# Performance work log

Measured on AMD Instinct MI355X. Metric: run time of the kernel, lower is better.

The kernel has to match this reference:

```python
import jax, jax.numpy as jnp
import numpy as np
from jax import lax

NEG = -1e9
B, H, C, TX, TY = 4, 256, 80, 256, 1024  # batch, hidden, mel bins, text len, mel len


def setup_inputs() -> dict:
    key = jax.random.key(0)
    k = jax.random.split(key, 6)
    en = jax.random.normal(k[0], (B, H, TX), jnp.float32)
    mu = jax.random.normal(k[1], (B, C, TX), jnp.float32)
    log_sigma = 0.1 * jax.random.normal(k[2], (B, C, TX), jnp.float32)
    y = jax.random.normal(k[3], (B, C, TY), jnp.float32)
    x_lengths = jax.random.randint(k[4], (B,), TX // 2, TX + 1, jnp.int32)
    y_lengths = jax.random.randint(k[5], (B,), TY // 2, TY + 1, jnp.int32)
    return {"en": en, "mu": mu, "log_sigma": log_sigma, "y": y,
            "x_lengths": x_lengths, "y_lengths": y_lengths}


def sequence_mask(lengths, max_len):
    return jnp.arange(max_len)[None, :] < lengths[:, None]


def compute_log_probs(mu, log_sigma, y):
    # y: [B,C,Ty] -> [B,1,Ty,C]; mu/log_sigma: [B,C,Tx] -> [B,Tx,1,C]
    yb = jnp.transpose(y, (0, 2, 1))[:, None]
    mub = jnp.transpose(mu, (0, 2, 1))[:, :, None]
    lsb = jnp.transpose(log_sigma, (0, 2, 1))[:, :, None]
    # mse / sigma^2 = (y-mu)^2 * exp(-2*log_sigma); mean over channel dim
    expo = -0.5 * jnp.mean((yb - mub) ** 2 * jnp.exp(-2.0 * lsb), axis=-1)  # [B,Tx,Ty]
    return expo - 0.5 * jnp.mean(lsb, axis=-1)  # broadcast [B,Tx,1] -> [B,Tx,Ty]


def maximum_path(logp, mask, x_lengths, y_lengths):
    """Monotonic alignment search (Glow-TTS Viterbi DP), vectorized over batch."""
    b, tx, ty = logp.shape
    lp = jnp.where(mask > 0, logp, NEG)
    cols = jnp.moveaxis(lp, 2, 0)  # [Ty, B, Tx]
    v0 = jnp.broadcast_to(jnp.where(jnp.arange(tx) == 0, 0.0, NEG), (b, tx)).astype(logp.dtype)

    def fwd(v, col):
        v_shift = jnp.concatenate([jnp.full((b, 1), NEG, v.dtype), v[:, :-1]], axis=1)
        diag = v_shift > v  # come from (x-1, y-1) rather than (x, y-1)
        return col + jnp.maximum(v, v_shift), diag

    _, diags = lax.scan(fwd, v0, cols)  # diags: [Ty, B, Tx] bool

    xs_idx = jnp.arange(tx)

    def bwd(idx, inp):
        yv, dcol = inp
        active = yv < y_lengths  # [B]
        row = (xs_idx[None, :] == idx[:, None]) & active[:, None]
        d = jnp.take_along_axis(dcol, idx[:, None], axis=1)[:, 0]
        idx = jnp.where(active & (idx > 0) & d, idx - 1, idx)
        return idx, row

    _, rows = lax.scan(bwd, x_lengths - 1, (jnp.arange(ty), diags), reverse=True)
    return lax.stop_gradient(jnp.moveaxis(rows, 0, 2).astype(logp.dtype))  # [B,Tx,Ty]


def generate_path(dr, mask):
    # dr: [B,Tx] durations; mask: [B,Tx,Ty]
    ty = mask.shape[-1]
    cum = jnp.cumsum(dr, axis=1)
    pm = (jnp.arange(ty)[None, None, :] < cum[:, :, None]).astype(dr.dtype)
    path = pm - jnp.pad(pm, ((0, 0), (1, 0), (0, 0)))[:, :-1]
    return path * mask


def reference(en, mu, log_sigma, y, x_lengths, y_lengths):
    tx, ty = mu.shape[-1], y.shape[-1]
    x_mask = sequence_mask(x_lengths, tx).astype(jnp.float32)  # [B,Tx]
    y_mask = sequence_mask(y_lengths, ty).astype(jnp.float32)  # [B,Ty]
    attn_mask = x_mask[:, :, None] * y_mask[:, None, :]        # [B,Tx,Ty]
    logp = compute_log_probs(mu, log_sigma, y)
    attn = maximum_path(logp, attn_mask, x_lengths, y_lengths)
    dr_mas = jnp.sum(attn, axis=-1)                            # durations [B,Tx]
    path = generate_path(dr_mas, attn_mask)                    # convert_dr_to_align
    # expand_encoder_outputs: attn^T @ en^T -> [B,H,Ty]
    o_en_ex = jnp.einsum('bxy,bhx->bhy', path, en)
    return o_en_ex, logp, attn, dr_mas
```

## Files before the change

kernel.cpp:

```cpp
#include <hip/hip_runtime.h>
#include <cstdint>
#include <cmath>

#define B_ 4
#define H_ 256
#define C_ 80
#define TX_ 256
#define TY_ 1024
#define NCH_ 32
#define NEGF (-1e9f)

#define OFF_LOGP (B_*H_*TY_)
#define OFF_ATTN (OFF_LOGP + B_*TX_*TY_)
#define OFF_DR   (OFF_ATTN + B_*TX_*TY_)

__device__ __forceinline__ float dpp_shr1_negfill_f32(float x) {
  union { float f; int i; } u, o, r;
  u.f = x; o.f = NEGF;
  r.i = __builtin_amdgcn_update_dpp(o.i, u.i, 0x138, 0xf, 0xf, false);
  return r.f;
}

__global__ __launch_bounds__(256) void k_logp(
    const float* __restrict__ mu, const float* __restrict__ ls,
    const float* __restrict__ y, const int* __restrict__ xlp,
    const int* __restrict__ ylp, float* __restrict__ logp_out,
    float* __restrict__ lpT)
{
  const int b  = blockIdx.y;
  const int x0 = blockIdx.x * 4;
  const int tid = threadIdx.x;
  __shared__ double s_w[4][C_];
  __shared__ double s_m1[4][C_];
  __shared__ double s_wm2[4][C_];
  __shared__ double s_lsv[4][C_];
  __shared__ double s_K[4];
  __shared__ double s_t0[4];
  __shared__ float tile[TY_][4];
  for (int i = tid; i < 4 * C_; i += 256) {
    int xi = i / C_, c = i - xi * C_;
    double m = (double)mu[(b * C_ + c) * TX_ + x0 + xi];
    double l = (double)ls[(b * C_ + c) * TX_ + x0 + xi];
    double w = exp(-2.0 * l);
    s_w[xi][c]   = w;
    s_m1[xi][c]  = -2.0 * w * m;
    s_wm2[xi][c] = w * m * m;
    s_lsv[xi][c] = l;
  }
  __syncthreads();
  {
    int xi = tid >> 6, cc = tid & 63;
    double kp = (cc < C_) ? s_wm2[xi][cc] : 0.0;
    double tp = (cc < C_) ? s_lsv[xi][cc] : 0.0;
    if (cc + 64 < C_) { kp += s_wm2[xi][cc + 64]; tp += s_lsv[xi][cc + 64]; }
#pragma unroll
    for (int off = 32; off; off >>= 1) {
      kp += __shfl_down(kp, off);
      tp += __shfl_down(tp, off);
    }
    if (cc == 0) { s_K[xi] = kp; s_t0[xi] = -0.5 * (tp * (1.0 / C_)); }
  }
  __syncthreads();

  const int t0 = tid * 4;
  double acc[4][4];
#pragma unroll
  for (int xi = 0; xi < 4; ++xi)
#pragma unroll
    for (int k = 0; k < 4; ++k) acc[xi][k] = 0.0;

  const float4* yp = (const float4*)(y + (size_t)b * C_ * TY_) + tid;
#pragma unroll 4
  for (int c = 0; c < C_; ++c) {
    float4 yv = yp[c * (TY_ / 4)];
    double y0 = yv.x, y1 = yv.y, y2 = yv.z, y3 = yv.w;
#pragma unroll
    for (int xi = 0; xi < 4; ++xi) {
      double w = s_w[xi][c], m1 = s_m1[xi][c];
      double u0 = fma(w, y0, m1), u1 = fma(w, y1, m1);
      double u2 = fma(w, y2, m1), u3 = fma(w, y3, m1);
      acc[xi][0] = fma(u0, y0, acc[xi][0]);
      acc[xi][1] = fma(u1, y1, acc[xi][1]);
      acc[xi][2] = fma(u2, y2, acc[xi][2]);
      acc[xi][3] = fma(u3, y3, acc[xi][3]);
    }
  }

  const int xlen = xlp[b], ylen = ylp[b];
#pragma unroll
  for (int xi = 0; xi < 4; ++xi) {
    int x = x0 + xi;
    double c0 = s_t0[xi], K = s_K[xi];
    float r[4];
#pragma unroll
    for (int k = 0; k < 4; ++k)
      r[k] = (float)((acc[xi][k] + K) * (-0.5 / C_) + c0);
    *(float4*)&logp_out[((size_t)(b * TX_ + x)) * TY_ + t0] =
        make_float4(r[0], r[1], r[2], r[3]);
    bool xm = x < xlen;
#pragma unroll
    for (int k = 0; k < 4; ++k)
      tile[t0 + k][xi] = (xm && (t0 + k) < ylen) ? r[k] : NEGF;
  }
  __syncthreads();

  float* dst = lpT + (size_t)b * TY_ * TX_ + x0;
  const float4* tp = (const float4*)tile;
#pragma unroll
  for (int k = 0; k < 4; ++k) {
    int t = tid + 256 * k;
    *(float4*)&dst[(size_t)t * TX_] = tp[t];
  }
}

#define PHASE_BAR() \
  asm volatile("s_waitcnt lgkmcnt(0)\n\ts_barrier" ::: "memory")

#define PHASEQ(FL, FC, q)                                                   \
  {                                                                         \
    const int cl = (q) - w;                                                 \
    const int clc = cl < 0 ? 0 : (cl >= NCH_ ? NCH_ - 1 : cl);              \
    const float* cb = gb + (size_t)clc * 32 * TX_ + tid;                    \
    _Pragma("unroll")                                                       \
    for (int i = 0; i < 32; ++i) FL[i] = cb[i * TX_];    \
    const int cc = (q) - 2 - w;                                             \
    if (cc >= 0 && cc < NCH_) {                                             \
      if (cc == 0) v = (tid == 0) ? 0.0f : NEGF;                            \
      uint32_t word = 0u;                                                   \
      const float* bp = &bdry[cc & 1][w][0];                                \
      float bv[32];                                                         \
      _Pragma("unroll")                                                     \
      for (int i = 0; i < 8; ++i)                                           \
        *(float4*)&bv[4 * i] = *(const float4*)(bp + 4 * i);                \
      float bs[32];                                                         \
      bs[0] = v;                                                            \
      _Pragma("unroll")                                                     \
      for (int i = 0; i < 32; ++i) {                                        \
        float vl = dpp_shr1_negfill_f32(v);                                 \
        if (amlane0) vl = bv[i];                                            \
        if (vl > v) word |= (1u << i);                                      \
        float nv = FC[i] + fmaxf(v, vl);                                    \
        if (i < 31) bs[i + 1] = nv;                                         \
        v = nv;                                                             \
      }                                                                     \
      if (lane == 63) {                                                     \
        float* wr = &bdry[cc & 1][w + 1][0];                                \
        _Pragma("unroll")                                                   \
        for (int i = 0; i < 8; ++i)                                         \
          *(float4*)(wr + 4 * i) = *(float4*)&bs[4 * i];                    \
      }                                                                     \
      bits[cc * 256 + tid] = word;                                          \
    }                                                                       \
    PHASE_BAR();                                                            \
  }

__global__ __launch_bounds__(256, 1) void k_dp(
    const float* __restrict__ lpT, const int* __restrict__ xlp,
    const int* __restrict__ ylp, float* __restrict__ dr_out,
    int* __restrict__ cum_ws, int* __restrict__ xt_ws)
{
  const int b = blockIdx.x;
  const int tid = threadIdx.x;
  const int lane = tid & 63;
  const int w = tid >> 6;
  __shared__ uint32_t bits[8192];
  __shared__ uint32_t dur[TX_];
  __shared__ float bdry[2][5][32];

  const float* gb = lpT + (size_t)b * TY_ * TX_;
  const bool amlane0 = (w > 0) && (lane == 0);

  float v = NEGF;
  float f0[32], f1[32], f2[32];

  for (int q = 0; q < 39; q += 3) {
    PHASEQ(f0, f1, q);
    PHASEQ(f1, f2, q + 1);
    PHASEQ(f2, f0, q + 2);
  }
  __syncthreads();

  dur[tid] = 0;
  __syncthreads();

  const int xlen = xlp[b], ylen = ylp[b];
  if (tid == 0) {
    int idx = xlen - 1;
    int t = ylen - 1;
    while (t >= 0) {
      if (idx == 0) { dur[0] = (uint32_t)(t + 1); break; }
      int ww = t >> 5, rr = t & 31;
      uint32_t w0 = bits[ww * 256 + idx];
      uint32_t w1 = (ww > 0) ? bits[(ww - 1) * 256 + idx] : 0u;
      w0 &= (rr == 31) ? 0xffffffffu : ((1u << (rr + 1)) - 1u);
      uint32_t wd = w0;
      int wsel = ww;
      if (wd == 0) { wd = w1; wsel = ww - 1; }
      while (wd == 0 && wsel > 0) { --wsel; wd = bits[wsel * 256 + idx]; }
      if (wd == 0) { dur[idx] = (uint32_t)(t + 1); break; }
      int bitpos = 31 - __builtin_clz(wd);
      int tp = (wsel << 5) | bitpos;
      dur[idx] = (uint32_t)(t - tp + 1);
      --idx;
      t = tp - 1;
    }
  }
  __syncthreads();

  if (w == 0) {
    uint32_t d0 = dur[4 * lane], d1 = dur[4 * lane + 1];
    uint32_t d2 = dur[4 * lane + 2], d3 = dur[4 * lane + 3];
    uint32_t own = d0 + d1 + d2 + d3;
    uint32_t s = own;
#pragma unroll
    for (int off = 1; off < 64; off <<= 1) {
      uint32_t n = __shfl_up(s, off);
      if (lane >= off) s += n;
    }
    uint32_t base = s - own;
    uint32_t c0 = base + d0, c1 = c0 + d1, c2 = c1 + d2, c3 = c2 + d3;
    int x = 4 * lane;
    cum_ws[b * TX_ + x]     = (int)c0;
    cum_ws[b * TX_ + x + 1] = (int)c1;
    cum_ws[b * TX_ + x + 2] = (int)c2;
    cum_ws[b * TX_ + x + 3] = (int)c3;
    dr_out[b * TX_ + x]     = (float)d0;
    dr_out[b * TX_ + x + 1] = (float)d1;
    dr_out[b * TX_ + x + 2] = (float)d2;
    dr_out[b * TX_ + x + 3] = (float)d3;
    int* xt = xt_ws + b * TY_;
    for (uint32_t t = c0 - d0; t < c0; ++t) xt[t] = x;
    for (uint32_t t = c1 - d1; t < c1; ++t) xt[t] = x + 1;
    for (uint32_t t = c2 - d2; t < c2; ++t) xt[t] = x + 2;
    for (uint32_t t = c3 - d3; t < c3; ++t) xt[t] = x + 3;
  }
}

__global__ __launch_bounds__(256) void k_epi(
    const int* __restrict__ cum_ws, const int* __restrict__ xt_ws,
    const float* __restrict__ en, const int* __restrict__ ylp,
    float* __restrict__ attn, float* __restrict__ oen)
{
  const int b = blockIdx.y, bx = blockIdx.x, tid = threadIdx.x;
  __shared__ float row[TX_];
  if (bx < TX_) {
    const int x = bx;
    int hi = cum_ws[b * TX_ + x];
    int lo = (x > 0) ? cum_ws[b * TX_ + x - 1] : 0;
    int t0 = tid * 4;
    float4 v;
    v.x = (t0     >= lo && t0     < hi) ? 1.f : 0.f;
    v.y = (t0 + 1 >= lo && t0 + 1 < hi) ? 1.f : 0.f;
    v.z = (t0 + 2 >= lo && t0 + 2 < hi) ? 1.f : 0.f;
    v.w = (t0 + 3 >= lo && t0 + 3 < hi) ? 1.f : 0.f;
    *(float4*)&attn[((size_t)(b * TX_ + x)) * TY_ + t0] = v;
  } else {
    const int h = bx - TX_;
    row[tid] = en[((size_t)(b * H_ + h)) * TX_ + tid];
    __syncthreads();
    const int ylen = ylp[b];
    int t0 = tid * 4;
    int4 xi = *(const int4*)&xt_ws[b * TY_ + t0];
    float4 v;
    v.x = (t0     < ylen) ? row[xi.x & (TX_ - 1)] : 0.f;
    v.y = (t0 + 1 < ylen) ? row[xi.y & (TX_ - 1)] : 0.f;
    v.z = (t0 + 2 < ylen) ? row[xi.z & (TX_ - 1)] : 0.f;
    v.w = (t0 + 3 < ylen) ? row[xi.w & (TX_ - 1)] : 0.f;
    *(float4*)&oen[((size_t)(b * H_ + h)) * TY_ + t0] = v;
  }
}

extern "C" void kernel_launch(void* const* d_in, const int* in_sizes, int n_in,
                              void* d_out, int out_size, void* d_ws, size_t ws_size,
                              hipStream_t stream)
{
  const float* en = (const float*)d_in[0];
  const float* mu = (const float*)d_in[1];
  const float* ls = (const float*)d_in[2];
  const float* y  = (const float*)d_in[3];
  const int*   xl = (const int*)d_in[4];
  const int*   yl = (const int*)d_in[5];

  float* out  = (float*)d_out;
  float* oen  = out;
  float* logp = out + OFF_LOGP;
  float* attn = out + OFF_ATTN;
  float* dr   = out + OFF_DR;

  int* cum = (int*)d_ws;
  int* xt  = cum + B_ * TX_;

  k_logp<<<dim3(TX_ / 4, B_),   256, 0, stream>>>(mu, ls, y, xl, yl, logp, attn);
  k_dp  <<<B_,                  256, 0, stream>>>(attn, xl, yl, dr, cum, xt);
  k_epi <<<dim3(TX_ + H_, B_),  256, 0, stream>>>(cum, xt, en, yl, attn, oen);
}
```

Measured before the change: 200.0 us.

## Halve DP wavefront chunk to 16 columns with inline-asm double-buffered prefetch

Reworks the Viterbi forward DP wavefront so each phase covers 16 time columns instead of 32, which shortens the pipeline fill and drain across the four wavefronts. Column loads are issued through inline-asm global_load into fixed VGPR banks v128-v159 as a two-deep prefetch, gated by an explicit vmcnt wait. Direction bits from two chunks are packed into one word. The cost is twice as many barriers, plus the risk that hard-coded register clobbers clash with what the compiler allocates.

```diff
diff --git a/kernel.cpp b/kernel.cpp
--- a/kernel.cpp
+++ b/kernel.cpp
@@ -7,7 +7,7 @@
 #define C_ 80
 #define TX_ 256
 #define TY_ 1024
-#define NCH_ 32
+#define NC_ 64
 #define NEGF (-1e9f)
 
 #define OFF_LOGP (B_*H_*TY_)
@@ -113,46 +113,48 @@
   }
 }
 
-#define PHASE_BAR() \
-  asm volatile("s_waitcnt lgkmcnt(0)\n\ts_barrier" ::: "memory")
-
-#define PHASEQ(FL, FC, q)                                                   \
-  {                                                                         \
-    const int cl = (q) - w;                                                 \
-    const int clc = cl < 0 ? 0 : (cl >= NCH_ ? NCH_ - 1 : cl);              \
-    const float* cb = gb + (size_t)clc * 32 * TX_ + tid;                    \
-    _Pragma("unroll")                                                       \
-    for (int i = 0; i < 32; ++i) FL[i] = cb[i * TX_];    \
-    const int cc = (q) - 2 - w;                                             \
-    if (cc >= 0 && cc < NCH_) {                                             \
-      if (cc == 0) v = (tid == 0) ? 0.0f : NEGF;                            \
-      uint32_t word = 0u;                                                   \
-      const float* bp = &bdry[cc & 1][w][0];                                \
-      float bv[32];                                                         \
-      _Pragma("unroll")                                                     \
-      for (int i = 0; i < 8; ++i)                                           \
-        *(float4*)&bv[4 * i] = *(const float4*)(bp + 4 * i);                \
-      float bs[32];                                                         \
-      bs[0] = v;                                                            \
-      _Pragma("unroll")                                                     \
-      for (int i = 0; i < 32; ++i) {                                        \
-        float vl = dpp_shr1_negfill_f32(v);                                 \
-        if (amlane0) vl = bv[i];                                            \
-        if (vl > v) word |= (1u << i);                                      \
-        float nv = FC[i] + fmaxf(v, vl);                                    \
-        if (i < 31) bs[i + 1] = nv;                                         \
-        v = nv;                                                             \
-      }                                                                     \
-      if (lane == 63) {                                                     \
-        float* wr = &bdry[cc & 1][w + 1][0];                                \
-        _Pragma("unroll")                                                   \
-        for (int i = 0; i < 8; ++i)                                         \
-          *(float4*)(wr + 4 * i) = *(float4*)&bs[4 * i];                    \
-      }                                                                     \
-      bits[cc * 256 + tid] = word;                                          \
-    }                                                                       \
-    PHASE_BAR();                                                            \
-  }
+#define BANKCLB \
+  "v128","v129","v130","v131","v132","v133","v134","v135", \
+  "v136","v137","v138","v139","v140","v141","v142","v143", \
+  "v144","v145","v146","v147","v148","v149","v150","v151", \
+  "v152","v153","v154","v155","v156","v157","v158","v159"
+
+#define ISSUE(R, base)                                                      \
+  asm volatile(                                                             \
+    "global_load_dword v[" #R "], %0, off\n\t"                              \
+    "global_load_dword v[" #R "+1], %0, off offset:1024\n\t"                \
+    "global_load_dword v[" #R "+2], %0, off offset:2048\n\t"                \
+    "global_load_dword v[" #R "+3], %0, off offset:3072\n\t"                \
+    "global_load_dword v[" #R "+4], %1, off\n\t"                            \
+    "global_load_dword v[" #R "+5], %1, off offset:1024\n\t"                \
+    "global_load_dword v[" #R "+6], %1, off offset:2048\n\t"                \
+    "global_load_dword v[" #R "+7], %1, off offset:3072\n\t"                \
+    "global_load_dword v[" #R "+8], %2, off\n\t"                            \
+    "global_load_dword v[" #R "+9], %2, off offset:1024\n\t"                \
+    "global_load_dword v[" #R "+10], %2, off offset:2048\n\t"               \
+    "global_load_dword v[" #R "+11], %2, off offset:3072\n\t"               \
+    "global_load_dword v[" #R "+12], %3, off\n\t"                           \
+    "global_load_dword v[" #R "+13], %3, off offset:1024\n\t"               \
+    "global_load_dword v[" #R "+14], %3, off offset:2048\n\t"               \
+    "global_load_dword v[" #R "+15], %3, off offset:3072\n\t"               \
+    :: "v"(base), "v"((base) + 4 * TX_), "v"((base) + 8 * TX_),             \
+       "v"((base) + 12 * TX_) : BANKCLB)
+
+#define COPYOUT(R, WAITSTR, cl)                                             \
+  asm volatile(WAITSTR                                                      \
+    "v_mov_b32 %0, v[" #R "]\n\t"   "v_mov_b32 %1, v[" #R "+1]\n\t"         \
+    "v_mov_b32 %2, v[" #R "+2]\n\t" "v_mov_b32 %3, v[" #R "+3]\n\t"         \
+    "v_mov_b32 %4, v[" #R "+4]\n\t" "v_mov_b32 %5, v[" #R "+5]\n\t"         \
+    "v_mov_b32 %6, v[" #R "+6]\n\t" "v_mov_b32 %7, v[" #R "+7]\n\t"         \
+    "v_mov_b32 %8, v[" #R "+8]\n\t" "v_mov_b32 %9, v[" #R "+9]\n\t"         \
+    "v_mov_b32 %10, v[" #R "+10]\n\t" "v_mov_b32 %11, v[" #R "+11]\n\t"     \
+    "v_mov_b32 %12, v[" #R "+12]\n\t" "v_mov_b32 %13, v[" #R "+13]\n\t"     \
+    "v_mov_b32 %14, v[" #R "+14]\n\t" "v_mov_b32 %15, v[" #R "+15]"         \
+    : "=v"((cl)[0]),  "=v"((cl)[1]),  "=v"((cl)[2]),  "=v"((cl)[3]),        \
+      "=v"((cl)[4]),  "=v"((cl)[5]),  "=v"((cl)[6]),  "=v"((cl)[7]),        \
+      "=v"((cl)[8]),  "=v"((cl)[9]),  "=v"((cl)[10]), "=v"((cl)[11]),       \
+      "=v"((cl)[12]), "=v"((cl)[13]), "=v"((cl)[14]), "=v"((cl)[15])        \
+    :: BANKCLB)
 
 __global__ __launch_bounds__(256, 1) void k_dp(
     const float* __restrict__ lpT, const int* __restrict__ xlp,
@@ -165,19 +167,61 @@
   const int w = tid >> 6;
   __shared__ uint32_t bits[8192];
   __shared__ uint32_t dur[TX_];
-  __shared__ float bdry[2][5][32];
-
-  const float* gb = lpT + (size_t)b * TY_ * TX_;
+  __shared__ float bdry[2][5][16];
+
+  const float* gb = lpT + (size_t)b * TY_ * TX_ + tid;
   const bool amlane0 = (w > 0) && (lane == 0);
 
   float v = NEGF;
-  float f0[32], f1[32], f2[32];
-
-  for (int q = 0; q < 39; q += 3) {
-    PHASEQ(f0, f1, q);
-    PHASEQ(f1, f2, q + 1);
-    PHASEQ(f2, f0, q + 2);
-  }
+  uint32_t word = 0;
+  float cl[16];
+
+  ISSUE(128, gb);
+  ISSUE(144, gb + 16 * TX_);
+
+  for (int q = 0; q < NC_ + 3; ++q) {
+    const int cc = q - w;
+    if (cc >= 0 && cc < NC_) {
+      if (cc & 1) {
+        COPYOUT(144, "s_waitcnt vmcnt(16)\n\t", cl);
+        const int nc = (cc + 2 < NC_) ? cc + 2 : NC_ - 1;
+        ISSUE(144, gb + nc * 16 * TX_);
+      } else {
+        COPYOUT(128, "s_waitcnt vmcnt(16)\n\t", cl);
+        const int nc = (cc + 2 < NC_) ? cc + 2 : NC_ - 1;
+        ISSUE(128, gb + nc * 16 * TX_);
+      }
+      if (cc == 0) { v = (tid == 0) ? 0.0f : NEGF; word = 0u; }
+      const uint32_t bitbase = 1u << ((cc & 1) << 4);
+      const float* bp = &bdry[cc & 1][w][0];
+      float bv[16];
+      *(float4*)&bv[0]  = *(const float4*)(bp);
+      *(float4*)&bv[4]  = *(const float4*)(bp + 4);
+      *(float4*)&bv[8]  = *(const float4*)(bp + 8);
+      *(float4*)&bv[12] = *(const float4*)(bp + 12);
+      float bs[16];
+      bs[0] = v;
+#pragma unroll
+      for (int i = 0; i < 16; ++i) {
+        float vl = dpp_shr1_negfill_f32(v);
+        if (amlane0) vl = bv[i];
+        if (vl > v) word |= (bitbase << i);
+        float nv = cl[i] + fmaxf(v, vl);
+        if (i < 15) bs[i + 1] = nv;
+        v = nv;
+      }
+      if (lane == 63) {
+        float* wr = &bdry[cc & 1][w + 1][0];
+        *(float4*)(wr)      = *(float4*)&bs[0];
+        *(float4*)(wr + 4)  = *(float4*)&bs[4];
+        *(float4*)(wr + 8)  = *(float4*)&bs[8];
+        *(float4*)(wr + 12) = *(float4*)&bs[12];
+      }
+      if (cc & 1) { bits[(cc >> 1) * 256 + tid] = word; word = 0u; }
+    }
+    asm volatile("s_waitcnt lgkmcnt(0)\n\ts_barrier" ::: "memory");
+  }
+  asm volatile("s_waitcnt vmcnt(0)" ::: "memory");
   __syncthreads();
 
   dur[tid] = 0;
```

After: 203.3 us. Within noise of the previous version (+1.7%).
